# Kernel optimization log

Measured on AMD Instinct MI355X. Metric: run time of the kernel, lower is better.

The kernel has to match this reference:

```python
import jax, jax.numpy as jnp
import numpy as np

IN_FEATURES = 4096
OUT_FEATURES = 4096
BATCH = 64


def setup_inputs() -> dict:
    key = jax.random.key(0)
    ks = jax.random.split(key, 7)
    rho_lo, rho_hi = -5.0, -3.0
    bound = 1.0 / np.sqrt(IN_FEATURES)
    x = jax.random.normal(ks[0], (BATCH, IN_FEATURES), dtype=jnp.float32)
    W_mu = jax.random.uniform(ks[1], (OUT_FEATURES, IN_FEATURES), minval=-bound, maxval=bound, dtype=jnp.float32)
    W_rho = jax.random.uniform(ks[2], (OUT_FEATURES, IN_FEATURES), minval=rho_lo, maxval=rho_hi, dtype=jnp.float32)
    b_mu = jax.random.uniform(ks[3], (OUT_FEATURES,), minval=-bound, maxval=bound, dtype=jnp.float32)
    b_rho = jax.random.uniform(ks[4], (OUT_FEATURES,), minval=rho_lo, maxval=rho_hi, dtype=jnp.float32)
    W_rand = jax.random.normal(ks[5], (OUT_FEATURES, IN_FEATURES), dtype=jnp.float32)
    b_rand = jax.random.normal(ks[6], (OUT_FEATURES,), dtype=jnp.float32)
    return {"x": x, "W_mu": W_mu, "W_rho": W_rho, "b_mu": b_mu, "b_rho": b_rho,
            "W_rand": W_rand, "b_rand": b_rand}


def reference(x, W_mu, W_rho, b_mu, b_rho, W_rand, b_rand):
    # std = logaddexp(0, rho) == softplus(rho); reparameterized sample
    W = W_mu + W_rand * jnp.logaddexp(0.0, W_rho)   # [out, in]
    b = b_mu + b_rand * jnp.logaddexp(0.0, b_rho)   # [out]
    # F.linear(x, W, b) = x @ W.T + b
    return jnp.einsum('bi,oi->bo', x, W) + b
```

## Files before the change

kernel.cpp:

```cpp
#include <hip/hip_runtime.h>
#include <hip/hip_bf16.h>

#define IN_F   4096
#define OUT_F  4096
#define BATCH  64
#define KSPLIT 16
#define KC     (IN_F / KSPLIT)
#define COLS_PER_BLOCK 64

typedef __attribute__((ext_vector_type(8))) short  bf16x8;
typedef __attribute__((ext_vector_type(4))) float  f32x4;

__device__ __forceinline__ float softplus_f(float r) {
    return fmaxf(r, 0.0f) + __logf(1.0f + __expf(-fabsf(r)));
}

__device__ __forceinline__ short bf16_of(float f) {
    union { float f; unsigned u; } v; v.f = f;
    unsigned r = v.u + 0x7FFFu + ((v.u >> 16) & 1u);
    return (short)(r >> 16);
}

__device__ __forceinline__ bf16x8 pack8(float w0, float w1, float w2, float w3,
                                        float w4, float w5, float w6, float w7) {
    bf16x8 b;
    b[0] = bf16_of(w0); b[1] = bf16_of(w1); b[2] = bf16_of(w2); b[3] = bf16_of(w3);
    b[4] = bf16_of(w4); b[5] = bf16_of(w5); b[6] = bf16_of(w6); b[7] = bf16_of(w7);
    return b;
}

__global__ __launch_bounds__(256, 2) void bayes_gemm(
    const float* __restrict__ x,
    const float* __restrict__ Wmu,
    const float* __restrict__ Wrho,
    const float* __restrict__ Wrnd,
    float* __restrict__ out)
{
    const int tid  = threadIdx.x;
    const int wave = tid >> 6;
    const int lane = tid & 63;
    const int nl   = lane & 15;
    const int kg   = lane >> 4;

    const int o     = blockIdx.x * COLS_PER_BLOCK + wave * 16 + nl;
    const int kBase = blockIdx.y * KC;

    const size_t woff = (size_t)o * IN_F + kBase + kg * 8;
    const float* pmu  = Wmu  + woff;
    const float* prho = Wrho + woff;
    const float* prnd = Wrnd + woff;
    const float* px   = x + (size_t)nl * IN_F + kBase + kg * 8;

    f32x4 acc0 = {0.f,0.f,0.f,0.f};
    f32x4 acc1 = {0.f,0.f,0.f,0.f};
    f32x4 acc2 = {0.f,0.f,0.f,0.f};
    f32x4 acc3 = {0.f,0.f,0.f,0.f};

    #pragma unroll 2
    for (int kk = 0; kk < KC; kk += 32) {
        const float4 mu0 = *(const float4*)(pmu);
        const float4 mu1 = *(const float4*)(pmu + 4);
        const float4 rh0 = *(const float4*)(prho);
        const float4 rh1 = *(const float4*)(prho + 4);
        const float4 rn0 = *(const float4*)(prnd);
        const float4 rn1 = *(const float4*)(prnd + 4);

        const bf16x8 bfrag = pack8(
            fmaf(rn0.x, softplus_f(rh0.x), mu0.x),
            fmaf(rn0.y, softplus_f(rh0.y), mu0.y),
            fmaf(rn0.z, softplus_f(rh0.z), mu0.z),
            fmaf(rn0.w, softplus_f(rh0.w), mu0.w),
            fmaf(rn1.x, softplus_f(rh1.x), mu1.x),
            fmaf(rn1.y, softplus_f(rh1.y), mu1.y),
            fmaf(rn1.z, softplus_f(rh1.z), mu1.z),
            fmaf(rn1.w, softplus_f(rh1.w), mu1.w));

        const float4 xa0 = *(const float4*)(px);
        const float4 xa1 = *(const float4*)(px + 4);
        const float4 xb0 = *(const float4*)(px + 16 * IN_F);
        const float4 xb1 = *(const float4*)(px + 16 * IN_F + 4);
        const float4 xc0 = *(const float4*)(px + 32 * IN_F);
        const float4 xc1 = *(const float4*)(px + 32 * IN_F + 4);
        const float4 xd0 = *(const float4*)(px + 48 * IN_F);
        const float4 xd1 = *(const float4*)(px + 48 * IN_F + 4);

        const bf16x8 a0 = pack8(xa0.x, xa0.y, xa0.z, xa0.w, xa1.x, xa1.y, xa1.z, xa1.w);
        const bf16x8 a1 = pack8(xb0.x, xb0.y, xb0.z, xb0.w, xb1.x, xb1.y, xb1.z, xb1.w);
        const bf16x8 a2 = pack8(xc0.x, xc0.y, xc0.z, xc0.w, xc1.x, xc1.y, xc1.z, xc1.w);
        const bf16x8 a3 = pack8(xd0.x, xd0.y, xd0.z, xd0.w, xd1.x, xd1.y, xd1.z, xd1.w);

        acc0 = __builtin_amdgcn_mfma_f32_16x16x32_bf16(a0, bfrag, acc0, 0, 0, 0);
        acc1 = __builtin_amdgcn_mfma_f32_16x16x32_bf16(a1, bfrag, acc1, 0, 0, 0);
        acc2 = __builtin_amdgcn_mfma_f32_16x16x32_bf16(a2, bfrag, acc2, 0, 0, 0);
        acc3 = __builtin_amdgcn_mfma_f32_16x16x32_bf16(a3, bfrag, acc3, 0, 0, 0);

        pmu += 32; prho += 32; prnd += 32; px += 32;
    }

    #pragma unroll
    for (int r = 0; r < 4; ++r) {
        const int mrow = kg * 4 + r;
        atomicAdd(&out[(size_t)(mrow     ) * OUT_F + o], acc0[r]);
        atomicAdd(&out[(size_t)(mrow + 16) * OUT_F + o], acc1[r]);
        atomicAdd(&out[(size_t)(mrow + 32) * OUT_F + o], acc2[r]);
        atomicAdd(&out[(size_t)(mrow + 48) * OUT_F + o], acc3[r]);
    }
}

__global__ __launch_bounds__(256) void bayes_bias(
    float* __restrict__ out,
    const float* __restrict__ bmu,
    const float* __restrict__ brho,
    const float* __restrict__ brnd)
{
    const int i4 = (blockIdx.x * 256 + threadIdx.x) * 4;
    float4 v = *(const float4*)(out + i4);
    const int o = i4 & (OUT_F - 1);
    v.x += fmaf(brnd[o    ], softplus_f(brho[o    ]), bmu[o    ]);
    v.y += fmaf(brnd[o + 1], softplus_f(brho[o + 1]), bmu[o + 1]);
    v.z += fmaf(brnd[o + 2], softplus_f(brho[o + 2]), bmu[o + 2]);
    v.w += fmaf(brnd[o + 3], softplus_f(brho[o + 3]), bmu[o + 3]);
    *(float4*)(out + i4) = v;
}

extern "C" void kernel_launch(void* const* d_in, const int* in_sizes, int n_in,
                              void* d_out, int out_size, void* d_ws, size_t ws_size,
                              hipStream_t stream) {
    const float* x     = (const float*)d_in[0];
    const float* Wmu   = (const float*)d_in[1];
    const float* Wrho  = (const float*)d_in[2];
    const float* bmu   = (const float*)d_in[3];
    const float* brho  = (const float*)d_in[4];
    const float* Wrnd  = (const float*)d_in[5];
    const float* brnd  = (const float*)d_in[6];
    float* out = (float*)d_out;

    hipMemsetAsync(out, 0, (size_t)BATCH * OUT_F * sizeof(float), stream);

    dim3 grid(OUT_F / COLS_PER_BLOCK, KSPLIT);
    bayes_gemm<<<grid, 256, 0, stream>>>(x, Wmu, Wrho, Wrnd, out);

    bayes_bias<<<(BATCH * OUT_F) / (256 * 4), 256, 0, stream>>>(out, bmu, brho, brnd);
}
```

Measured before the change: 223.0 us.

## Fuse bias into GEMM with in-block K reduction, drop atomics and memset

```diff
diff --git a/kernel.cpp b/kernel.cpp
--- a/kernel.cpp
+++ b/kernel.cpp
@@ -4,9 +4,8 @@
 #define IN_F   4096
 #define OUT_F  4096
 #define BATCH  64
-#define KSPLIT 16
-#define KC     (IN_F / KSPLIT)
-#define COLS_PER_BLOCK 64
+#define NWAVE  8
+#define NITER  (IN_F / (NWAVE*32))
 
 typedef __attribute__((ext_vector_type(8))) short  bf16x8;
 typedef __attribute__((ext_vector_type(4))) float  f32x4;
@@ -29,98 +28,109 @@
     return b;
 }
 
-__global__ __launch_bounds__(256, 2) void bayes_gemm(
+#define LD4(p) (*(const float4*)(p))
+
+__global__ __launch_bounds__(512, 2) void bayes_fused(
     const float* __restrict__ x,
     const float* __restrict__ Wmu,
     const float* __restrict__ Wrho,
     const float* __restrict__ Wrnd,
+    const float* __restrict__ bmu,
+    const float* __restrict__ brho,
+    const float* __restrict__ brnd,
     float* __restrict__ out)
 {
+    __shared__ float red[NWAVE][BATCH][17];
+
     const int tid  = threadIdx.x;
     const int wave = tid >> 6;
     const int lane = tid & 63;
     const int nl   = lane & 15;
     const int kg   = lane >> 4;
 
-    const int o     = blockIdx.x * COLS_PER_BLOCK + wave * 16 + nl;
-    const int kBase = blockIdx.y * KC;
+    const int colbase = blockIdx.x * 16;
+    const int o  = colbase + nl;
+    const int k0 = wave * 32 + kg * 8;
 
-    const size_t woff = (size_t)o * IN_F + kBase + kg * 8;
-    const float* pmu  = Wmu  + woff;
-    const float* prho = Wrho + woff;
-    const float* prnd = Wrnd + woff;
-    const float* px   = x + (size_t)nl * IN_F + kBase + kg * 8;
+    const float* pmu  = Wmu  + (size_t)o * IN_F + k0;
+    const float* prho = Wrho + (size_t)o * IN_F + k0;
+    const float* prnd = Wrnd + (size_t)o * IN_F + k0;
+    const float* px   = x    + (size_t)nl * IN_F + k0;
 
     f32x4 acc0 = {0.f,0.f,0.f,0.f};
     f32x4 acc1 = {0.f,0.f,0.f,0.f};
     f32x4 acc2 = {0.f,0.f,0.f,0.f};
     f32x4 acc3 = {0.f,0.f,0.f,0.f};
 
-    #pragma unroll 2
-    for (int kk = 0; kk < KC; kk += 32) {
-        const float4 mu0 = *(const float4*)(pmu);
-        const float4 mu1 = *(const float4*)(pmu + 4);
-        const float4 rh0 = *(const float4*)(prho);
-        const float4 rh1 = *(const float4*)(prho + 4);
-        const float4 rn0 = *(const float4*)(prnd);
-        const float4 rn1 = *(const float4*)(prnd + 4);
+    float4 cm0 = LD4(pmu),      cm1 = LD4(pmu + 4);
+    float4 cr0 = LD4(prho),     cr1 = LD4(prho + 4);
+    float4 cn0 = LD4(prnd),     cn1 = LD4(prnd + 4);
+    float4 xA0 = LD4(px),                xA1 = LD4(px + 4);
+    float4 xB0 = LD4(px + 16*IN_F),      xB1 = LD4(px + 16*IN_F + 4);
+    float4 xC0 = LD4(px + 32*IN_F),      xC1 = LD4(px + 32*IN_F + 4);
+    float4 xD0 = LD4(px + 48*IN_F),      xD1 = LD4(px + 48*IN_F + 4);
+
+    #pragma unroll
+    for (int it = 0; it < NITER; ++it) {
+        pmu += NWAVE*32; prho += NWAVE*32; prnd += NWAVE*32; px += NWAVE*32;
+
+        float4 nm0 = cm0, nm1 = cm1, nr0 = cr0, nr1 = cr1, nn0 = cn0, nn1 = cn1;
+        float4 yA0 = xA0, yA1 = xA1, yB0 = xB0, yB1 = xB1;
+        float4 yC0 = xC0, yC1 = xC1, yD0 = xD0, yD1 = xD1;
+        if (it + 1 < NITER) {
+            nm0 = LD4(pmu);      nm1 = LD4(pmu + 4);
+            nr0 = LD4(prho);     nr1 = LD4(prho + 4);
+            nn0 = LD4(prnd);     nn1 = LD4(prnd + 4);
+            yA0 = LD4(px);               yA1 = LD4(px + 4);
+            yB0 = LD4(px + 16*IN_F);     yB1 = LD4(px + 16*IN_F + 4);
+            yC0 = LD4(px + 32*IN_F);     yC1 = LD4(px + 32*IN_F + 4);
+            yD0 = LD4(px + 48*IN_F);     yD1 = LD4(px + 48*IN_F + 4);
+        }
 
         const bf16x8 bfrag = pack8(
-            fmaf(rn0.x, softplus_f(rh0.x), mu0.x),
-            fmaf(rn0.y, softplus_f(rh0.y), mu0.y),
-            fmaf(rn0.z, softplus_f(rh0.z), mu0.z),
-            fmaf(rn0.w, softplus_f(rh0.w), mu0.w),
-            fmaf(rn1.x, softplus_f(rh1.x), mu1.x),
-            fmaf(rn1.y, softplus_f(rh1.y), mu1.y),
-            fmaf(rn1.z, softplus_f(rh1.z), mu1.z),
-            fmaf(rn1.w, softplus_f(rh1.w), mu1.w));
+            fmaf(cn0.x, softplus_f(cr0.x), cm0.x),
+            fmaf(cn0.y, softplus_f(cr0.y), cm0.y),
+            fmaf(cn0.z, softplus_f(cr0.z), cm0.z),
+            fmaf(cn0.w, softplus_f(cr0.w), cm0.w),
+            fmaf(cn1.x, softplus_f(cr1.x), cm1.x),
+            fmaf(cn1.y, softplus_f(cr1.y), cm1.y),
+            fmaf(cn1.z, softplus_f(cr1.z), cm1.z),
+            fmaf(cn1.w, softplus_f(cr1.w), cm1.w));
 
-        const float4 xa0 = *(const float4*)(px);
-        const float4 xa1 = *(const float4*)(px + 4);
-        const float4 xb0 = *(const float4*)(px + 16 * IN_F);
-        const float4 xb1 = *(const float4*)(px + 16 * IN_F + 4);
-        const float4 xc0 = *(const float4*)(px + 32 * IN_F);
-        const float4 xc1 = *(const float4*)(px + 32 * IN_F + 4);
-        const float4 xd0 = *(const float4*)(px + 48 * IN_F);
-        const float4 xd1 = *(const float4*)(px + 48 * IN_F + 4);
-
-        const bf16x8 a0 = pack8(xa0.x, xa0.y, xa0.z, xa0.w, xa1.x, xa1.y, xa1.z, xa1.w);
-        const bf16x8 a1 = pack8(xb0.x, xb0.y, xb0.z, xb0.w, xb1.x, xb1.y, xb1.z, xb1.w);
-        const bf16x8 a2 = pack8(xc0.x, xc0.y, xc0.z, xc0.w, xc1.x, xc1.y, xc1.z, xc1.w);
-        const bf16x8 a3 = pack8(xd0.x, xd0.y, xd0.z, xd0.w, xd1.x, xd1.y, xd1.z, xd1.w);
+        const bf16x8 a0 = pack8(xA0.x,xA0.y,xA0.z,xA0.w, xA1.x,xA1.y,xA1.z,xA1.w);
+        const bf16x8 a1 = pack8(xB0.x,xB0.y,xB0.z,xB0.w, xB1.x,xB1.y,xB1.z,xB1.w);
+        const bf16x8 a2 = pack8(xC0.x,xC0.y,xC0.z,xC0.w, xC1.x,xC1.y,xC1.z,xC1.w);
+        const bf16x8 a3 = pack8(xD0.x,xD0.y,xD0.z,xD0.w, xD1.x,xD1.y,xD1.z,xD1.w);
 
         acc0 = __builtin_amdgcn_mfma_f32_16x16x32_bf16(a0, bfrag, acc0, 0, 0, 0);
         acc1 = __builtin_amdgcn_mfma_f32_16x16x32_bf16(a1, bfrag, acc1, 0, 0, 0);
         acc2 = __builtin_amdgcn_mfma_f32_16x16x32_bf16(a2, bfrag, acc2, 0, 0, 0);
         acc3 = __builtin_amdgcn_mfma_f32_16x16x32_bf16(a3, bfrag, acc3, 0, 0, 0);
 
-        pmu += 32; prho += 32; prnd += 32; px += 32;
+        cm0=nm0; cm1=nm1; cr0=nr0; cr1=nr1; cn0=nn0; cn1=nn1;
+        xA0=yA0; xA1=yA1; xB0=yB0; xB1=yB1; xC0=yC0; xC1=yC1; xD0=yD0; xD1=yD1;
     }
 
     #pragma unroll
     for (int r = 0; r < 4; ++r) {
-        const int mrow = kg * 4 + r;
-        atomicAdd(&out[(size_t)(mrow     ) * OUT_F + o], acc0[r]);
-        atomicAdd(&out[(size_t)(mrow + 16) * OUT_F + o], acc1[r]);
-        atomicAdd(&out[(size_t)(mrow + 32) * OUT_F + o], acc2[r]);
-        atomicAdd(&out[(size_t)(mrow + 48) * OUT_F + o], acc3[r]);
+        red[wave][ 0 + kg*4 + r][nl] = acc0[r];
+        red[wave][16 + kg*4 + r][nl] = acc1[r];
+        red[wave][32 + kg*4 + r][nl] = acc2[r];
+        red[wave][48 + kg*4 + r][nl] = acc3[r];
     }
-}
+    __syncthreads();
 
-__global__ __launch_bounds__(256) void bayes_bias(
-    float* __restrict__ out,
-    const float* __restrict__ bmu,
-    const float* __restrict__ brho,
-    const float* __restrict__ brnd)
-{
-    const int i4 = (blockIdx.x * 256 + threadIdx.x) * 4;
-    float4 v = *(const float4*)(out + i4);
-    const int o = i4 & (OUT_F - 1);
-    v.x += fmaf(brnd[o    ], softplus_f(brho[o    ]), bmu[o    ]);
-    v.y += fmaf(brnd[o + 1], softplus_f(brho[o + 1]), bmu[o + 1]);
-    v.z += fmaf(brnd[o + 2], softplus_f(brho[o + 2]), bmu[o + 2]);
-    v.w += fmaf(brnd[o + 3], softplus_f(brho[o + 3]), bmu[o + 3]);
-    *(float4*)(out + i4) = v;
+    #pragma unroll
+    for (int e = tid; e < BATCH*16; e += 512) {
+        const int b = e >> 4;
+        const int c = e & 15;
+        float s = 0.f;
+        #pragma unroll
+        for (int w = 0; w < NWAVE; ++w) s += red[w][b][c];
+        const int oc = colbase + c;
+        s += fmaf(brnd[oc], softplus_f(brho[oc]), bmu[oc]);
+        out[(size_t)b * OUT_F + oc] = s;
+    }
 }
 
 extern "C" void kernel_launch(void* const* d_in, const int* in_sizes, int n_in,
@@ -135,10 +145,5 @@
     const float* brnd  = (const float*)d_in[6];
     float* out = (float*)d_out;
 
-    hipMemsetAsync(out, 0, (size_t)BATCH * OUT_F * sizeof(float), stream);
-
-    dim3 grid(OUT_F / COLS_PER_BLOCK, KSPLIT);
-    bayes_gemm<<<grid, 256, 0, stream>>>(x, Wmu, Wrho, Wrnd, out);
-
-    bayes_bias<<<(BATCH * OUT_F) / (256 * 4), 256, 0, stream>>>(out, bmu, brho, brnd);
+    bayes_fused<<<OUT_F/16, 512, 0, stream>>>(x, Wmu, Wrho, Wrnd, bmu, brho, brnd, out);
 }
```

Measured after the change: 223.0 us. No clear change (-0.0%).
